# Optimization experiments

Measured on AMD Instinct MI355X. Metric: run time of the kernel, lower is better.

The kernel has to match this reference:

```python
import jax, jax.numpy as jnp
import numpy as np

TAU = 0.8
ALPHA = 0.1
N_CLASSES = 100


def _normalize(x, axis=-1, eps=1e-12):
    # Matches torch.nn.functional.normalize (L2, eps clamp)
    return x / jnp.maximum(jnp.linalg.norm(x, axis=axis, keepdims=True), eps)


def setup_inputs() -> dict:
    key = jax.random.key(0)
    k1, k2, k3, k4 = jax.random.split(key, 4)
    bs, C, H, W = 32, 512, 14, 14
    m_sz = 16384
    queries = jax.random.normal(k1, (bs, C, H, W), dtype=jnp.float32)
    targets = jax.random.randint(k2, (bs,), 0, N_CLASSES)
    m_keys = _normalize(jax.random.normal(k3, (m_sz, C), dtype=jnp.float32))
    m_vals = jax.random.randint(k4, (m_sz,), 0, N_CLASSES).astype(jnp.int32)
    return {"queries": queries, "targets": targets, "m_keys": m_keys, "m_vals": m_vals}


def reference(queries, targets, m_keys, m_vals):
    # Eval-mode forward of Memory (upd_memory/use_centroid side effects excluded):
    # per-sample key similarity matmul + top-1 retrieval + masked triplet margin loss,
    # fully batched instead of the original python loop over the batch.
    bs, C, H, W = queries.shape
    n_hw = H * W
    q = queries.reshape(bs, C, n_hw).transpose(0, 2, 1)      # [bs, n_hw, C]
    q = _normalize(q, axis=-1)
    sims = jnp.einsum('bnc,mc->bnm', q, m_keys)               # [bs, n_hw, m_sz]

    # nearest memory slot per spatial location, then majority vote over locations
    nearest_val = m_vals[jnp.argmax(sims, axis=-1)]           # [bs, n_hw]
    counts = jnp.sum(nearest_val[:, :, None] == jnp.arange(N_CLASSES)[None, None, :],
                     axis=1)                                   # [bs, N_CLASSES]
    fetched_vals = jnp.argmax(counts, axis=-1).astype(jnp.int32)

    # masked pos/neg nearest similarities (mask by multiply, as in the original)
    correct = (m_vals[None, :] == targets[:, None])           # [bs, m_sz]
    pos = jnp.max(sims * correct[:, None, :], axis=-1)        # [bs, n_hw]
    neg = jnp.max(sims * (~correct)[:, None, :], axis=-1)     # [bs, n_hw]
    has_pos = jnp.any(correct, axis=-1)                       # [bs]
    per_loc = jnp.where(has_pos[:, None],
                        jax.nn.relu(neg - pos + ALPHA),
                        jax.nn.relu(neg + ALPHA))
    memory_loss = jnp.sum(jnp.mean(per_loc, axis=-1))         # sum over batch of per-sample means
    return fetched_vals, memory_loss
```

## Files before the change

### kernel.cpp

```cpp
#include <hip/hip_runtime.h>
#include <hip/hip_bf16.h>
#include <math.h>

typedef __attribute__((ext_vector_type(8))) short short8b;
typedef __attribute__((ext_vector_type(4))) float f32x4;

#define BSZ 32
#define NHW 196
#define M_ROWS 6272
#define MPAD 6400
#define CDIM 512
#define MSZ 16384
#define NCLS 100
#define ALPHA 0.1f
#define RSTR 67

__global__ __launch_bounds__(256) void k_invnorm4(const float* __restrict__ q,
                                                  float* __restrict__ ssq4,
                                                  int* __restrict__ gcount) {
    int b = blockIdx.x, cc = blockIdx.y, n = threadIdx.x;
    if (b == 0 && cc == 0) { gcount[n] = 0; gcount[256 + n] = 0; }
    if (n >= NHW) return;
    const float* base = q + ((size_t)b * CDIM + cc * 128) * NHW + n;
    float ss = 0.f;
#pragma unroll 8
    for (int c = 0; c < 128; ++c) { float v = base[(size_t)c * NHW]; ss = fmaf(v, v, ss); }
    ssq4[(size_t)(b * NHW + n) * 4 + cc] = ss;
}

__global__ __launch_bounds__(256) void k_decomp_q(
    const float* __restrict__ Q, const float* __restrict__ ssq4,
    unsigned short* __restrict__ qhi, float* __restrict__ qn)
{
    __shared__ unsigned short lh[32][65];
    __shared__ float fs[32][65];
    const int t = threadIdx.x;
    const int rb = blockIdx.x % 100, kb = blockIdx.x / 100;
    const int r0 = rb * 64, c0 = kb * 32;
    const int cin = t >> 6, rin = t & 63;
    const int r = r0 + rin;
    float iv = 0.f;
    if (r < M_ROWS) {
        const float4 s4 = *reinterpret_cast<const float4*>(ssq4 + (size_t)r * 4);
        iv = 1.f / fmaxf(sqrtf((s4.x + s4.y) + (s4.z + s4.w)), 1e-12f);
    }
    const int b = r / NHW, n = r - b * NHW;
#pragma unroll
    for (int ci = 0; ci < 8; ++ci) {
        int cl = ci * 4 + cin;
        float x = 0.f;
        if (r < M_ROWS) x = Q[((size_t)(b * CDIM + (c0 + cl))) * NHW + n] * iv;
        __hip_bfloat16 h = __float2bfloat16(x);
        lh[cl][rin] = *(unsigned short*)&h;
        fs[cl][rin] = x;
    }
    __syncthreads();
    const int r2 = t >> 2, seg = t & 3;
    short8b vh;
    float4 f0, f1;
#pragma unroll
    for (int i = 0; i < 8; ++i) vh[i] = (short)lh[seg * 8 + i][r2];
    f0.x = fs[seg * 8 + 0][r2]; f0.y = fs[seg * 8 + 1][r2];
    f0.z = fs[seg * 8 + 2][r2]; f0.w = fs[seg * 8 + 3][r2];
    f1.x = fs[seg * 8 + 4][r2]; f1.y = fs[seg * 8 + 5][r2];
    f1.z = fs[seg * 8 + 6][r2]; f1.w = fs[seg * 8 + 7][r2];
    size_t off = ((size_t)kb * MPAD + r0 + r2) * 32 + seg * 8;
    *(short8b*)(qhi + off) = vh;
    float* qb = qn + (size_t)(r0 + r2) * CDIM + c0 + seg * 8;
    *reinterpret_cast<float4*>(qb) = f0;
    *reinterpret_cast<float4*>(qb + 4) = f1;
}

__global__ __launch_bounds__(256) void k_decomp_k(
    const float* __restrict__ K, unsigned short* __restrict__ khi)
{
    int tid = blockIdx.x * 256 + threadIdx.x;
    int c4 = tid & 127, key = tid >> 7;
    int c = c4 << 2;
    const float4 v = *reinterpret_cast<const float4*>(K + (size_t)key * CDIM + c);
    float xs[4] = {v.x, v.y, v.z, v.w};
    unsigned short hs[4];
#pragma unroll
    for (int i = 0; i < 4; ++i) {
        __hip_bfloat16 h = __float2bfloat16(xs[i]);
        hs[i] = *(unsigned short*)&h;
    }
    size_t off = ((size_t)(c >> 5) * MSZ + key) * 32 + (c & 31);
    ushort4 H; H.x = hs[0]; H.y = hs[1]; H.z = hs[2]; H.w = hs[3];
    *reinterpret_cast<ushort4*>(khi + off) = H;
}

__device__ __forceinline__ void gload16(const void* g, void* lds) {
    __builtin_amdgcn_global_load_lds((const __attribute__((address_space(1))) void*)g,
                                     (__attribute__((address_space(3))) void*)lds,
                                     16, 0, 0);
}

__global__ __launch_bounds__(256, 4) void k_mfma(
    const unsigned short* __restrict__ qhi, const unsigned short* __restrict__ khi,
    const int* __restrict__ mvals, const int* __restrict__ tgt,
    float* __restrict__ pmax32, float* __restrict__ ppos, float* __restrict__ pneg)
{
    __shared__ __align__(16) float red[128 * RSTR];
    __shared__ int mv_s[128];
    char* smem = (char*)red;

    const int tid = threadIdx.x;
    const int w = tid >> 6, l = tid & 63;

    const int xcd = blockIdx.x & 7;
    const int idx = blockIdx.x >> 3;
    const int mt = idx >> 4;
    const int nt = (xcd << 4) | (idx & 15);
    const int r0 = mt * 128, n0 = nt * 128;

    const int srow = l >> 2;
    const int sg8 = (((l & 3) ^ ((l >> 3) & 3)) << 3);
    const int fr = l & 15;
    const int abyte = (fr << 6) + ((((l >> 4) ^ ((l >> 1) & 3))) << 4);

    const int wm = w >> 1, wn = w & 1;
    const int arow0 = wm * 64, bcol0 = wn * 64;

    f32x4 acc[4][4];
    const f32x4 zero4 = {0.f, 0.f, 0.f, 0.f};
#pragma unroll
    for (int m = 0; m < 4; ++m)
#pragma unroll
        for (int n = 0; n < 4; ++n) acc[m][n] = zero4;

    if (tid < 128) mv_s[tid] = mvals[n0 + tid];

    for (int ks = 0; ks < 8; ++ks) {
        __syncthreads();
#pragma unroll
        for (int h = 0; h < 2; ++h) {
            const int kb = 2 * ks + h;
            const size_t qb = ((size_t)kb * MPAD + r0) * 32;
            const size_t ko = ((size_t)kb * MSZ + n0) * 32;
#pragma unroll
            for (int j = 0; j < 2; ++j) {
                const int rr = w * 32 + j * 16 + srow;
                const int dst = h * 8192 + w * 2048 + j * 1024;
                gload16(qhi + qb + (size_t)rr * 32 + sg8, smem + dst);
                gload16(khi + ko + (size_t)rr * 32 + sg8, smem + 16384 + dst);
            }
        }
        __syncthreads();
#pragma unroll
        for (int h = 0; h < 2; ++h) {
            const char* bq = smem + h * 8192;
            const char* bk = smem + 16384 + h * 8192;
            short8b bh[4], ah[4];
#pragma unroll
            for (int n = 0; n < 4; ++n)
                bh[n] = *(const short8b*)(bk + ((bcol0 + n * 16) << 6) + abyte);
#pragma unroll
            for (int m = 0; m < 4; ++m)
                ah[m] = *(const short8b*)(bq + ((arow0 + m * 16) << 6) + abyte);
#pragma unroll
            for (int m = 0; m < 4; ++m)
#pragma unroll
                for (int n = 0; n < 4; ++n)
                    acc[m][n] = __builtin_amdgcn_mfma_f32_16x16x32_bf16(ah[m], bh[n], acc[m][n], 0, 0, 0);
        }
    }
    __syncthreads();

    const int s0 = r0 / NHW;
    int s1 = (r0 + 127) / NHW; if (s1 > 31) s1 = 31;
    const int tg0 = tgt[s0], tg1 = tgt[s1];
    bool c0m[4], c1m[4];
#pragma unroll
    for (int n = 0; n < 4; ++n) {
        const int cl = bcol0 + n * 16 + fr;
        c0m[n] = (mv_s[cl] == tg0);
        c1m[n] = (mv_s[cl] == tg1);
    }

#pragma unroll
    for (int m = 0; m < 4; ++m) {
#pragma unroll
        for (int rg = 0; rg < 4; ++rg) {
            const int rloc = arow0 + m * 16 + ((l >> 4) << 2) + rg;
            const int rglob = r0 + rloc;
            int samp = rglob / NHW; samp = samp > 31 ? 31 : samp;
            const bool use0 = (samp == s0);
            float p = -INFINITY, ng = -INFINITY;
#pragma unroll
            for (int n = 0; n < 4; ++n) {
                const float v = acc[m][n][rg];
                const bool corr = use0 ? c0m[n] : c1m[n];
                p  = fmaxf(p,  corr ? v : 0.f);
                ng = fmaxf(ng, corr ? 0.f : v);
            }
            red[rloc * RSTR + (wn << 4) + fr] = p;
            red[rloc * RSTR + 34 + (wn << 4) + fr] = ng;
        }
    }
    __syncthreads();
    {
        const int row = tid & 127;
        const int base = row * RSTR + ((tid < 128) ? 0 : 34);
        float v = red[base];
#pragma unroll 31
        for (int i = 1; i < 32; ++i) v = fmaxf(v, red[base + i]);
        if (tid < 128) ppos[(size_t)nt * MPAD + r0 + row] = v;
        else           pneg[(size_t)nt * MPAD + r0 + row] = v;
    }
    __syncthreads();

#pragma unroll
    for (int m = 0; m < 4; ++m) {
#pragma unroll
        for (int rg = 0; rg < 4; ++rg) {
            const int rloc = arow0 + m * 16 + ((l >> 4) << 2) + rg;
            const float vh0 = fmaxf(acc[m][0][rg], acc[m][1][rg]);
            const float vh1 = fmaxf(acc[m][2][rg], acc[m][3][rg]);
            red[rloc * RSTR + (wn << 5) + fr] = vh0;
            red[rloc * RSTR + (wn << 5) + 16 + fr] = vh1;
        }
    }
    __syncthreads();
#pragma unroll
    for (int uu = 0; uu < 2; ++uu) {
        const int u = tid + uu * 256;
        const int row = u >> 2, grp = u & 3;
        const int base = row * RSTR + (grp << 4);
        float v = red[base];
#pragma unroll 15
        for (int i = 1; i < 16; ++i) v = fmaxf(v, red[base + i]);
        pmax32[(size_t)(r0 + row) * 512 + (nt << 2) + grp] = v;
    }
}

__global__ __launch_bounds__(256) void k_plan(
    const float* __restrict__ pmax32,
    int* __restrict__ gcount, unsigned short* __restrict__ gtasks,
    unsigned long long* __restrict__ packed)
{
    __shared__ float redm[4];
    const int row = blockIdx.x, t = threadIdx.x;
    const float m0 = pmax32[(size_t)row * 512 + t];
    const float m1 = pmax32[(size_t)row * 512 + 256 + t];
    float m = fmaxf(m0, m1);
#pragma unroll
    for (int off = 1; off < 64; off <<= 1) m = fmaxf(m, __shfl_xor(m, off));
    if ((t & 63) == 0) redm[t >> 6] = m;
    __syncthreads();
    const float M = fmaxf(fmaxf(redm[0], redm[1]), fmaxf(redm[2], redm[3]));
    const float thr = M - 0.010f;
    if (t == 0) packed[row] = 0ull;
    if (m0 >= thr) {
        int s = atomicAdd(&gcount[t], 1);
        gtasks[(size_t)t * M_ROWS + s] = (unsigned short)row;
    }
    if (m1 >= thr) {
        int s = atomicAdd(&gcount[256 + t], 1);
        gtasks[(size_t)(256 + t) * M_ROWS + s] = (unsigned short)row;
    }
}

__device__ __forceinline__ unsigned long long enc_vi(float v, int idx) {
    unsigned u = __float_as_uint(v);
    u = (u & 0x80000000u) ? ~u : (u | 0x80000000u);
    return ((unsigned long long)u << 32) | (unsigned)(0xFFFFFFFFu - (unsigned)idx);
}

__global__ __launch_bounds__(256, 2) void k_redot(
    const float* __restrict__ qn, const float* __restrict__ mk,
    const int* __restrict__ gcount, const unsigned short* __restrict__ gtasks,
    unsigned long long* __restrict__ packed)
{
    __shared__ float ks[32][516];
    __shared__ float qrow[512];
    __shared__ float part[32][9];
    const int g = blockIdx.x, t = threadIdx.x;
    const int cnt = gcount[g];
    if (cnt == 0) return;
    {
        const float4* src = reinterpret_cast<const float4*>(mk + (size_t)g * 32 * CDIM);
        for (int i = t; i < 4096; i += 256) {
            const int key = i >> 7, pos = i & 127;
            *reinterpret_cast<float4*>(&ks[key][pos << 2]) = src[i];
        }
    }
    const int kj = t & 31, seg = t >> 5;
    for (int i = 0; i < cnt; ++i) {
        const int row = gtasks[(size_t)g * M_ROWS + i];
        *reinterpret_cast<float2*>(&qrow[t * 2]) =
            *reinterpret_cast<const float2*>(qn + (size_t)row * CDIM + t * 2);
        __syncthreads();
        float s = 0.f;
        const float4* kr = reinterpret_cast<const float4*>(&ks[kj][seg * 64]);
        const float4* qr = reinterpret_cast<const float4*>(&qrow[seg * 64]);
#pragma unroll
        for (int u = 0; u < 16; ++u) {
            const float4 a = qr[u], b = kr[u];
            s = fmaf(a.x, b.x, s); s = fmaf(a.y, b.y, s);
            s = fmaf(a.z, b.z, s); s = fmaf(a.w, b.w, s);
        }
        part[kj][seg] = s;
        __syncthreads();
        if (t < 32) {
            float sim = ((part[t][0] + part[t][1]) + (part[t][2] + part[t][3]))
                      + ((part[t][4] + part[t][5]) + (part[t][6] + part[t][7]));
            int ki = g * 32 + t;
#pragma unroll
            for (int off = 1; off < 32; off <<= 1) {
                const float ov = __shfl_xor(sim, off);
                const int   oi = __shfl_xor(ki, off);
                if (ov > sim || (ov == sim && oi < ki)) { sim = ov; ki = oi; }
            }
            if (t == 0)
                atomicMax((unsigned long long*)&packed[row], enc_vi(sim, ki));
        }
        __syncthreads();
    }
}

__global__ __launch_bounds__(256) void k_merge(
    const int* __restrict__ mvals, const int* __restrict__ tgt,
    const unsigned long long* __restrict__ packed,
    const float* __restrict__ ppos, const float* __restrict__ pneg,
    float* __restrict__ out, float* __restrict__ means)
{
    __shared__ int counts[NCLS];
    __shared__ float perloc[256];
    __shared__ int haspos;
    const int b = blockIdx.x, t = threadIdx.x;
    if (t == 0) haspos = 0;
    if (t < NCLS) counts[t] = 0;
    perloc[t] = 0.f;
    __syncthreads();
    const int tg = tgt[b];
    int found = 0;
    for (int i = t; i < MSZ; i += 256) found |= (mvals[i] == tg) ? 1 : 0;
    if (found) atomicOr(&haspos, 1);
    __syncthreads();
    if (t < NHW) {
        const int row = b * NHW + t;
        float p = -INFINITY, ng = -INFINITY;
        for (int c = 0; c < 128; ++c) {
            p  = fmaxf(p,  ppos[(size_t)c * MPAD + row]);
            ng = fmaxf(ng, pneg[(size_t)c * MPAD + row]);
        }
        const int ri = (int)(0xFFFFFFFFu - (unsigned)(packed[row] & 0xFFFFFFFFull));
        atomicAdd(&counts[mvals[ri]], 1);
        perloc[t] = haspos ? fmaxf(ng - p + ALPHA, 0.f)
                           : fmaxf(ng + ALPHA, 0.f);
    }
    __syncthreads();
    for (int s = 128; s > 0; s >>= 1) {
        if (t < s) perloc[t] += perloc[t + s];
        __syncthreads();
    }
    if (t == 0) {
        int bestc = 0, bestn = counts[0];
        for (int c = 1; c < NCLS; ++c)
            if (counts[c] > bestn) { bestn = counts[c]; bestc = c; }
        out[b] = (float)bestc;
        means[b] = perloc[0] / (float)NHW;
    }
}

__global__ __launch_bounds__(64) void k_final(const float* __restrict__ means,
                                              float* __restrict__ out) {
    if (threadIdx.x == 0) {
        float s = 0.f;
        for (int b = 0; b < BSZ; ++b) s += means[b];
        out[BSZ] = s;
    }
}

#define BM 128
#define BN 128
#define BK 16
#define LDA (BM + 4)
#define LDB (BN + 4)

__global__ __launch_bounds__(256) void k_invnorm(const float* __restrict__ q,
                                                 float* __restrict__ invq) {
    int b = blockIdx.x, n = threadIdx.x;
    if (n >= NHW) return;
    const float* base = q + (size_t)b * CDIM * NHW + n;
    float ss = 0.f;
#pragma unroll 4
    for (int c = 0; c < CDIM; ++c) { float v = base[(size_t)c * NHW]; ss = fmaf(v, v, ss); }
    invq[b * NHW + n] = 1.f / fmaxf(sqrtf(ss), 1e-12f);
}

__global__ __launch_bounds__(256) void k_gemm_reduce(
    const float* __restrict__ Q, const float* __restrict__ Kz,
    const int* __restrict__ mvals, const int* __restrict__ tgt,
    const float* __restrict__ invq,
    float* __restrict__ pmax, int* __restrict__ pidx,
    float* __restrict__ ppos, float* __restrict__ pneg)
{
    __shared__ float As[BK][LDA];
    __shared__ float Bs[BK][LDB];
    __shared__ float run_max[BM];
    __shared__ int   run_idx[BM];
    __shared__ float run_pos[BM];
    __shared__ float run_neg[BM];
    __shared__ int   mv_s[BN];
    __shared__ int   tgt_s[BM];
    __shared__ float inv_s[BM];

    const int t = threadIdx.x;
    const int rt = blockIdx.x % 49;
    const int chunk = blockIdx.x / 49;
    const int r0 = rt * BM;

    if (t < BM) {
        run_max[t] = -INFINITY; run_idx[t] = 0;
        run_pos[t] = -INFINITY; run_neg[t] = -INFINITY;
        int row = r0 + t;
        tgt_s[t] = tgt[row / NHW];
        inv_s[t] = invq[row];
    }
    const int ty = t >> 4, tx = t & 15;
    __syncthreads();

    for (int tile = 0; tile < 8; ++tile) {
        const int key0 = chunk * 1024 + tile * BN;
        if (t < BN) mv_s[t] = mvals[key0 + t];
        float acc[8][8];
#pragma unroll
        for (int i = 0; i < 8; ++i)
#pragma unroll
            for (int j = 0; j < 8; ++j) acc[i][j] = 0.f;

        for (int ks = 0; ks < 32; ++ks) {
            const int c0 = ks * BK;
            __syncthreads();
#pragma unroll
            for (int it = 0; it < 2; ++it) {
                int i = t + it * 256;
                int k = i >> 5;
                int r4 = (i & 31) << 2;
                int row = r0 + r4;
                int b = row / NHW;
                int n = row - b * NHW;
                const float4 v = *reinterpret_cast<const float4*>(
                    Q + ((size_t)(b * CDIM + c0 + k)) * NHW + n);
                float4 w;
                w.x = v.x * inv_s[r4 + 0]; w.y = v.y * inv_s[r4 + 1];
                w.z = v.z * inv_s[r4 + 2]; w.w = v.w * inv_s[r4 + 3];
                *reinterpret_cast<float4*>(&As[k][r4]) = w;
            }
#pragma unroll
            for (int it = 0; it < 2; ++it) {
                int i = t + it * 256;
                int key = i >> 2;
                int cc = (i & 3) << 2;
                const float4 v = *reinterpret_cast<const float4*>(
                    Kz + (size_t)(key0 + key) * CDIM + c0 + cc);
                Bs[cc + 0][key] = v.x; Bs[cc + 1][key] = v.y;
                Bs[cc + 2][key] = v.z; Bs[cc + 3][key] = v.w;
            }
            __syncthreads();
#pragma unroll
            for (int k = 0; k < BK; ++k) {
                float4 a0 = *reinterpret_cast<const float4*>(&As[k][4 * ty]);
                float4 a1 = *reinterpret_cast<const float4*>(&As[k][64 + 4 * ty]);
                float4 b0 = *reinterpret_cast<const float4*>(&Bs[k][4 * tx]);
                float4 b1 = *reinterpret_cast<const float4*>(&Bs[k][64 + 4 * tx]);
                float a[8] = {a0.x, a0.y, a0.z, a0.w, a1.x, a1.y, a1.z, a1.w};
                float bb[8] = {b0.x, b0.y, b0.z, b0.w, b1.x, b1.y, b1.z, b1.w};
#pragma unroll
                for (int i = 0; i < 8; ++i)
#pragma unroll
                    for (int j = 0; j < 8; ++j)
                        acc[i][j] = fmaf(a[i], bb[j], acc[i][j]);
            }
        }
#pragma unroll
        for (int i = 0; i < 8; ++i) {
            int rl = (i < 4) ? (4 * ty + i) : (64 + 4 * ty + i - 4);
            int tgti = tgt_s[rl];
            float vmax = -INFINITY; int vidx = 0;
            float p = -INFINITY, ng = -INFINITY;
#pragma unroll
            for (int j = 0; j < 8; ++j) {
                int cl = (j < 4) ? (4 * tx + j) : (64 + 4 * tx + j - 4);
                float v = acc[i][j];
                int gk = key0 + cl;
                if (v > vmax) { vmax = v; vidx = gk; }
                bool corr = (mv_s[cl] == tgti);
                p  = fmaxf(p,  corr ? v : 0.f);
                ng = fmaxf(ng, corr ? 0.f : v);
            }
#pragma unroll
            for (int off = 1; off < 16; off <<= 1) {
                float om = __shfl_xor(vmax, off, 16);
                int   oi = __shfl_xor(vidx, off, 16);
                float op = __shfl_xor(p,    off, 16);
                float on = __shfl_xor(ng,   off, 16);
                if (om > vmax || (om == vmax && oi < vidx)) { vmax = om; vidx = oi; }
                p = fmaxf(p, op); ng = fmaxf(ng, on);
            }
            if (tx == 0) {
                if (vmax > run_max[rl]) { run_max[rl] = vmax; run_idx[rl] = vidx; }
                run_pos[rl] = fmaxf(run_pos[rl], p);
                run_neg[rl] = fmaxf(run_neg[rl], ng);
            }
        }
        __syncthreads();
    }
    if (t < BM) {
        int row = r0 + t;
        size_t o = (size_t)row * 16 + chunk;
        pmax[o] = run_max[t]; pidx[o] = run_idx[t];
        ppos[o] = run_pos[t]; pneg[o] = run_neg[t];
    }
}

__global__ __launch_bounds__(256) void k_merge_fb(
    const int* __restrict__ mvals, const int* __restrict__ tgt,
    const float* __restrict__ pmax, const int* __restrict__ pidx,
    const float* __restrict__ ppos, const float* __restrict__ pneg,
    float* __restrict__ out, float* __restrict__ means, int nch)
{
    __shared__ int counts[NCLS];
    __shared__ float perloc[256];
    __shared__ int haspos;
    const int b = blockIdx.x, t = threadIdx.x;
    if (t == 0) haspos = 0;
    if (t < NCLS) counts[t] = 0;
    perloc[t] = 0.f;
    __syncthreads();
    const int tg = tgt[b];
    int found = 0;
    for (int i = t; i < MSZ; i += 256) found |= (mvals[i] == tg) ? 1 : 0;
    if (found) atomicOr(&haspos, 1);
    __syncthreads();
    if (t < NHW) {
        int row = b * NHW + t;
        float vmax = -INFINITY; int vidx = 0;
        float p = -INFINITY, ng = -INFINITY;
        for (int c = 0; c < nch; ++c) {
            size_t o = (size_t)row * nch + c;
            float m = pmax[o]; int i_ = pidx[o];
            if (m > vmax || (m == vmax && i_ < vidx)) { vmax = m; vidx = i_; }
            p = fmaxf(p, ppos[o]); ng = fmaxf(ng, pneg[o]);
        }
        atomicAdd(&counts[mvals[vidx]], 1);
        perloc[t] = haspos ? fmaxf(ng - p + ALPHA, 0.f)
                           : fmaxf(ng + ALPHA, 0.f);
    }
    __syncthreads();
    for (int s = 128; s > 0; s >>= 1) {
        if (t < s) perloc[t] += perloc[t + s];
        __syncthreads();
    }
    if (t == 0) {
        int bestc = 0, bestn = counts[0];
        for (int c = 1; c < NCLS; ++c)
            if (counts[c] > bestn) { bestn = counts[c]; bestc = c; }
        out[b] = (float)bestc;
        means[b] = perloc[0] / (float)NHW;
    }
}

extern "C" void kernel_launch(void* const* d_in, const int* in_sizes, int n_in,
                              void* d_out, int out_size, void* d_ws, size_t ws_size,
                              hipStream_t stream) {
    const float* q  = (const float*)d_in[0];
    const int*   tg = (const int*)d_in[1];
    const float* mk = (const float*)d_in[2];
    const int*   mv = (const int*)d_in[3];
    float* out = (float*)d_out;

    unsigned short* khi = (unsigned short*)d_ws;
    unsigned short* qhi = khi + (size_t)MSZ * CDIM;
    float* qn     = (float*)(qhi + (size_t)MPAD * CDIM);
    float* ssq4   = qn + (size_t)MPAD * CDIM;
    float* pmax32 = ssq4 + (size_t)M_ROWS * 4;
    float* ppos   = pmax32 + (size_t)MPAD * 512;
    float* pneg   = ppos + (size_t)MPAD * 128;
    int*   gcount = (int*)(pneg + (size_t)MPAD * 128);
    unsigned short* gtasks = (unsigned short*)(gcount + 512);
    unsigned long long* packed = (unsigned long long*)(gtasks + (size_t)512 * M_ROWS);
    float* means  = (float*)(packed + M_ROWS);
    size_t need = (size_t)((char*)(means + BSZ) - (char*)d_ws);

    if (ws_size >= need) {
        k_invnorm4<<<dim3(BSZ, 4), 256, 0, stream>>>(q, ssq4, gcount);
        k_decomp_q<<<1600, 256, 0, stream>>>(q, ssq4, qhi, qn);
        k_decomp_k<<<(MSZ * 128) / 256, 256, 0, stream>>>(mk, khi);
        k_mfma<<<6400, 256, 0, stream>>>(qhi, khi, mv, tg, pmax32, ppos, pneg);
        k_plan<<<M_ROWS, 256, 0, stream>>>(pmax32, gcount, gtasks, packed);
        k_redot<<<512, 256, 0, stream>>>(qn, mk, gcount, gtasks, packed);
        k_merge<<<BSZ, 256, 0, stream>>>(mv, tg, packed, ppos, pneg, out, means);
        k_final<<<1, 64, 0, stream>>>(means, out);
    } else {
        float* invq0  = (float*)d_ws;
        float* pmax0  = invq0 + M_ROWS;
        float* ppos0  = pmax0 + (size_t)M_ROWS * 16;
        float* pneg0  = ppos0 + (size_t)M_ROWS * 16;
        int*   pidx0  = (int*)(pneg0 + (size_t)M_ROWS * 16);
        float* means0 = (float*)(pidx0 + (size_t)M_ROWS * 16);
        k_invnorm<<<BSZ, 256, 0, stream>>>(q, invq0);
        k_gemm_reduce<<<49 * 16, 256, 0, stream>>>(q, mk, mv, tg, invq0,
                                                   pmax0, pidx0, ppos0, pneg0);
        k_merge_fb<<<BSZ, 256, 0, stream>>>(mv, tg, pmax0, pidx0, ppos0, pneg0, out, means0, 16);
        k_final<<<1, 64, 0, stream>>>(means0, out);
    }
}
```

Measured before the change: 248.1 us.

## Shrink MFMA kernel LDS to raise occupancy and merge prep kernels

Cuts the GEMM kernel's shared memory from about 34KB to 32KB by reducing the epilogue in two 64-row halves. It also moves the m_vals lookups into registers, which lets launch bounds rise from 4 to 5 blocks per CU. Separately, the q-norm kernel and the key bf16 conversion kernel are fused into one launch to save launch overhead. The costs are extra barriers in the epilogue and possible register pressure or spills under the tighter launch bound.

```diff
diff --git a/kernel.cpp b/kernel.cpp
--- a/kernel.cpp
+++ b/kernel.cpp
@@ -15,17 +15,36 @@
 #define ALPHA 0.1f
 #define RSTR 67
 
-__global__ __launch_bounds__(256) void k_invnorm4(const float* __restrict__ q,
-                                                  float* __restrict__ ssq4,
-                                                  int* __restrict__ gcount) {
-    int b = blockIdx.x, cc = blockIdx.y, n = threadIdx.x;
-    if (b == 0 && cc == 0) { gcount[n] = 0; gcount[256 + n] = 0; }
-    if (n >= NHW) return;
-    const float* base = q + ((size_t)b * CDIM + cc * 128) * NHW + n;
-    float ss = 0.f;
+__global__ __launch_bounds__(256) void k_prep(
+    const float* __restrict__ q, float* __restrict__ ssq4, int* __restrict__ gcount,
+    const float* __restrict__ K, unsigned short* __restrict__ khi)
+{
+    const int bid = blockIdx.x;
+    if (bid < 128) {
+        const int b = bid >> 2, cc = bid & 3, n = threadIdx.x;
+        if (bid == 0) { gcount[n] = 0; gcount[256 + n] = 0; }
+        if (n >= NHW) return;
+        const float* base = q + ((size_t)b * CDIM + cc * 128) * NHW + n;
+        float ss = 0.f;
 #pragma unroll 8
-    for (int c = 0; c < 128; ++c) { float v = base[(size_t)c * NHW]; ss = fmaf(v, v, ss); }
-    ssq4[(size_t)(b * NHW + n) * 4 + cc] = ss;
+        for (int c = 0; c < 128; ++c) { float v = base[(size_t)c * NHW]; ss = fmaf(v, v, ss); }
+        ssq4[(size_t)(b * NHW + n) * 4 + cc] = ss;
+    } else {
+        const int tid = (bid - 128) * 256 + threadIdx.x;
+        const int c4 = tid & 127, key = tid >> 7;
+        const int c = c4 << 2;
+        const float4 v = *reinterpret_cast<const float4*>(K + (size_t)key * CDIM + c);
+        float xs[4] = {v.x, v.y, v.z, v.w};
+        unsigned short hs[4];
+#pragma unroll
+        for (int i = 0; i < 4; ++i) {
+            __hip_bfloat16 h = __float2bfloat16(xs[i]);
+            hs[i] = *(unsigned short*)&h;
+        }
+        size_t off = ((size_t)(c >> 5) * MSZ + key) * 32 + (c & 31);
+        ushort4 H; H.x = hs[0]; H.y = hs[1]; H.z = hs[2]; H.w = hs[3];
+        *reinterpret_cast<ushort4*>(khi + off) = H;
+    }
 }
 
 __global__ __launch_bounds__(256) void k_decomp_q(
@@ -71,39 +90,19 @@
     *reinterpret_cast<float4*>(qb + 4) = f1;
 }
 
-__global__ __launch_bounds__(256) void k_decomp_k(
-    const float* __restrict__ K, unsigned short* __restrict__ khi)
-{
-    int tid = blockIdx.x * 256 + threadIdx.x;
-    int c4 = tid & 127, key = tid >> 7;
-    int c = c4 << 2;
-    const float4 v = *reinterpret_cast<const float4*>(K + (size_t)key * CDIM + c);
-    float xs[4] = {v.x, v.y, v.z, v.w};
-    unsigned short hs[4];
-#pragma unroll
-    for (int i = 0; i < 4; ++i) {
-        __hip_bfloat16 h = __float2bfloat16(xs[i]);
-        hs[i] = *(unsigned short*)&h;
-    }
-    size_t off = ((size_t)(c >> 5) * MSZ + key) * 32 + (c & 31);
-    ushort4 H; H.x = hs[0]; H.y = hs[1]; H.z = hs[2]; H.w = hs[3];
-    *reinterpret_cast<ushort4*>(khi + off) = H;
-}
-
 __device__ __forceinline__ void gload16(const void* g, void* lds) {
     __builtin_amdgcn_global_load_lds((const __attribute__((address_space(1))) void*)g,
                                      (__attribute__((address_space(3))) void*)lds,
                                      16, 0, 0);
 }
 
-__global__ __launch_bounds__(256, 4) void k_mfma(
+__global__ __launch_bounds__(256, 5) void k_mfma(
     const unsigned short* __restrict__ qhi, const unsigned short* __restrict__ khi,
     const int* __restrict__ mvals, const int* __restrict__ tgt,
     float* __restrict__ pmax32, float* __restrict__ ppos, float* __restrict__ pneg)
 {
-    __shared__ __align__(16) float red[128 * RSTR];
-    __shared__ int mv_s[128];
-    char* smem = (char*)red;
+    __shared__ __align__(16) char smem[32768];
+    float* red = (float*)smem;
 
     const int tid = threadIdx.x;
     const int w = tid >> 6, l = tid & 63;
@@ -122,14 +121,16 @@
     const int wm = w >> 1, wn = w & 1;
     const int arow0 = wm * 64, bcol0 = wn * 64;
 
+    int mvv[4];
+#pragma unroll
+    for (int n = 0; n < 4; ++n) mvv[n] = mvals[n0 + bcol0 + n * 16 + fr];
+
     f32x4 acc[4][4];
     const f32x4 zero4 = {0.f, 0.f, 0.f, 0.f};
 #pragma unroll
     for (int m = 0; m < 4; ++m)
 #pragma unroll
         for (int n = 0; n < 4; ++n) acc[m][n] = zero4;
-
-    if (tid < 128) mv_s[tid] = mvals[n0 + tid];
 
     for (int ks = 0; ks < 8; ++ks) {
         __syncthreads();
@@ -173,64 +174,74 @@
     bool c0m[4], c1m[4];
 #pragma unroll
     for (int n = 0; n < 4; ++n) {
-        const int cl = bcol0 + n * 16 + fr;
-        c0m[n] = (mv_s[cl] == tg0);
-        c1m[n] = (mv_s[cl] == tg1);
-    }
-
-#pragma unroll
-    for (int m = 0; m < 4; ++m) {
-#pragma unroll
-        for (int rg = 0; rg < 4; ++rg) {
-            const int rloc = arow0 + m * 16 + ((l >> 4) << 2) + rg;
-            const int rglob = r0 + rloc;
-            int samp = rglob / NHW; samp = samp > 31 ? 31 : samp;
-            const bool use0 = (samp == s0);
-            float p = -INFINITY, ng = -INFINITY;
-#pragma unroll
-            for (int n = 0; n < 4; ++n) {
-                const float v = acc[m][n][rg];
-                const bool corr = use0 ? c0m[n] : c1m[n];
-                p  = fmaxf(p,  corr ? v : 0.f);
-                ng = fmaxf(ng, corr ? 0.f : v);
-            }
-            red[rloc * RSTR + (wn << 4) + fr] = p;
-            red[rloc * RSTR + 34 + (wn << 4) + fr] = ng;
-        }
-    }
-    __syncthreads();
-    {
-        const int row = tid & 127;
-        const int base = row * RSTR + ((tid < 128) ? 0 : 34);
-        float v = red[base];
+        c0m[n] = (mvv[n] == tg0);
+        c1m[n] = (mvv[n] == tg1);
+    }
+
+#pragma unroll
+    for (int b = 0; b < 2; ++b) {
+        if (wm == b) {
+#pragma unroll
+            for (int m = 0; m < 4; ++m) {
+#pragma unroll
+                for (int rg = 0; rg < 4; ++rg) {
+                    const int rloc = arow0 + m * 16 + ((l >> 4) << 2) + rg;
+                    const int rglob = r0 + rloc;
+                    int samp = rglob / NHW; samp = samp > 31 ? 31 : samp;
+                    const bool use0 = (samp == s0);
+                    float p = -INFINITY, ng = -INFINITY;
+#pragma unroll
+                    for (int n = 0; n < 4; ++n) {
+                        const float v = acc[m][n][rg];
+                        const bool corr = use0 ? c0m[n] : c1m[n];
+                        p  = fmaxf(p,  corr ? v : 0.f);
+                        ng = fmaxf(ng, corr ? 0.f : v);
+                    }
+                    const int rb = rloc & 63;
+                    red[rb * RSTR + (wn << 4) + fr] = p;
+                    red[rb * RSTR + 34 + (wn << 4) + fr] = ng;
+                }
+            }
+        }
+        __syncthreads();
+        if (tid < 128) {
+            const int row = tid & 63;
+            const int base = row * RSTR + ((tid < 64) ? 0 : 34);
+            float v = red[base];
 #pragma unroll 31
-        for (int i = 1; i < 32; ++i) v = fmaxf(v, red[base + i]);
-        if (tid < 128) ppos[(size_t)nt * MPAD + r0 + row] = v;
-        else           pneg[(size_t)nt * MPAD + r0 + row] = v;
-    }
-    __syncthreads();
-
-#pragma unroll
-    for (int m = 0; m < 4; ++m) {
-#pragma unroll
-        for (int rg = 0; rg < 4; ++rg) {
-            const int rloc = arow0 + m * 16 + ((l >> 4) << 2) + rg;
-            const float vh0 = fmaxf(acc[m][0][rg], acc[m][1][rg]);
-            const float vh1 = fmaxf(acc[m][2][rg], acc[m][3][rg]);
-            red[rloc * RSTR + (wn << 5) + fr] = vh0;
-            red[rloc * RSTR + (wn << 5) + 16 + fr] = vh1;
-        }
-    }
-    __syncthreads();
-#pragma unroll
-    for (int uu = 0; uu < 2; ++uu) {
-        const int u = tid + uu * 256;
-        const int row = u >> 2, grp = u & 3;
-        const int base = row * RSTR + (grp << 4);
-        float v = red[base];
+            for (int i = 1; i < 32; ++i) v = fmaxf(v, red[base + i]);
+            if (tid < 64) ppos[(size_t)nt * MPAD + r0 + b * 64 + row] = v;
+            else          pneg[(size_t)nt * MPAD + r0 + b * 64 + row] = v;
+        }
+        __syncthreads();
+    }
+
+#pragma unroll
+    for (int b = 0; b < 2; ++b) {
+        if (wm == b) {
+#pragma unroll
+            for (int m = 0; m < 4; ++m) {
+#pragma unroll
+                for (int rg = 0; rg < 4; ++rg) {
+                    const int rloc = arow0 + m * 16 + ((l >> 4) << 2) + rg;
+                    const int rb = rloc & 63;
+                    const float vh0 = fmaxf(acc[m][0][rg], acc[m][1][rg]);
+                    const float vh1 = fmaxf(acc[m][2][rg], acc[m][3][rg]);
+                    red[rb * RSTR + (wn << 5) + fr] = vh0;
+                    red[rb * RSTR + (wn << 5) + 16 + fr] = vh1;
+                }
+            }
+        }
+        __syncthreads();
+        {
+            const int row = tid >> 2, grp = tid & 3;
+            const int base = row * RSTR + (grp << 4);
+            float v = red[base];
 #pragma unroll 15
-        for (int i = 1; i < 16; ++i) v = fmaxf(v, red[base + i]);
-        pmax32[(size_t)(r0 + row) * 512 + (nt << 2) + grp] = v;
+            for (int i = 1; i < 16; ++i) v = fmaxf(v, red[base + i]);
+            pmax32[(size_t)(r0 + b * 64 + row) * 512 + (nt << 2) + grp] = v;
+        }
+        __syncthreads();
     }
 }
 
@@ -586,9 +597,8 @@
     size_t need = (size_t)((char*)(means + BSZ) - (char*)d_ws);
 
     if (ws_size >= need) {
-        k_invnorm4<<<dim3(BSZ, 4), 256, 0, stream>>>(q, ssq4, gcount);
+        k_prep<<<128 + (MSZ * 128) / 256, 256, 0, stream>>>(q, ssq4, gcount, mk, khi);
         k_decomp_q<<<1600, 256, 0, stream>>>(q, ssq4, qhi, qn);
-        k_decomp_k<<<(MSZ * 128) / 256, 256, 0, stream>>>(mk, khi);
         k_mfma<<<6400, 256, 0, stream>>>(qhi, khi, mv, tg, pmax32, ppos, pneg);
         k_plan<<<M_ROWS, 256, 0, stream>>>(pmax32, gcount, gtasks, packed);
         k_redot<<<512, 256, 0, stream>>>(qn, mk, gcount, gtasks, packed);
```

New measurement: 327.4 us. 1.32x slower.
